# Performance work log

Measured on AMD Instinct MI355X. Metric: run time of the kernel, lower is better.

The kernel has to match this reference:

```python
import jax, jax.numpy as jnp
import numpy as np

BN_EPS = 1e-5

def tanhshrink(x):
    return x - jnp.tanh(x)

def setup_inputs() -> dict:
    key = jax.random.key(0)
    ks = jax.random.split(key, 10)
    B, C, H, W = 32, 128, 32, 32
    RIN, RH, OC = 256, 512, 128
    s = lambda k, shape, fan: jax.random.normal(k, shape, dtype=jnp.float32) * (1.0 / np.sqrt(fan))
    return {
        "x": jax.random.normal(ks[0], (B, C, H, W), dtype=jnp.float32),
        "gamma": jnp.ones((C,), jnp.float32),
        "beta": jnp.zeros((C,), jnp.float32),
        "w_in": s(ks[1], (RIN, C), C),
        "b_in": jnp.zeros((RIN,), jnp.float32),
        "w_ih": s(ks[2], (RH, RIN), RIN),
        "b_ih": jnp.zeros((RH,), jnp.float32),
        "w_hh": s(ks[3], (RH, RH), RH),
        "b_hh": jnp.zeros((RH,), jnp.float32),
        "w_out": s(ks[4], (OC, RH), RH),
        "b_out": jnp.zeros((OC,), jnp.float32),
    }

def reference(x, gamma, beta, w_in, b_in, w_ih, b_ih, w_hh, b_hh, w_out, b_out):
    B, C, H, W = x.shape
    RH = w_hh.shape[0]
    # BatchNorm2d (training mode: batch statistics, biased variance)
    mean = jnp.mean(x, axis=(0, 2, 3), keepdims=True)
    var = jnp.var(x, axis=(0, 2, 3), keepdims=True)
    xn = (x - mean) * jax.lax.rsqrt(var + BN_EPS)
    xn = xn * gamma[None, :, None, None] + beta[None, :, None, None]
    # (B, L, C) sequence of flattened spatial locations
    seq = jnp.transpose(xn, (0, 2, 3, 1)).reshape(B, H * W, C)
    # Per-timestep Linear + Tanhshrink: has no recurrence, batch it over L
    inp = tanhshrink(jnp.einsum('blc,ic->bli', seq, w_in) + b_in)  # (B, L, RIN)
    # Precompute input contribution to RNNCell for all steps
    xgate = jnp.einsum('bli,hi->blh', inp, w_ih) + b_ih + b_hh  # (B, L, RH)
    xgate_t = jnp.transpose(xgate, (1, 0, 2))  # (L, B, RH)

    def step(h, xg):
        h_new = jnp.tanh(xg + h @ w_hh.T)
        return h_new, h_new

    h0 = jnp.zeros((B, RH), x.dtype)
    _, hs = jax.lax.scan(step, h0, xgate_t)  # (L, B, RH)
    outputs = jnp.transpose(hs, (1, 0, 2))  # (B, L, RH)
    out_seq = jnp.einsum('blh,oh->blo', outputs, w_out) + b_out  # (B, L, OC)
    out = jnp.transpose(out_seq.reshape(B, H, W, -1), (0, 3, 1, 2))
    return out
```

## Files before the change

kernel.cpp:

```cpp
#include <hip/hip_runtime.h>
#include <hip/hip_fp16.h>

typedef _Float16 f16;
typedef _Float16 f16x2 __attribute__((ext_vector_type(2)));
typedef _Float16 f16x8 __attribute__((ext_vector_type(8)));
typedef float    f32x4 __attribute__((ext_vector_type(4)));
typedef unsigned int u32;
typedef unsigned long long u64;

#define BN_EPS 1e-5f

static constexpr int BB  = 32;
static constexpr int CC  = 128;
static constexpr int HWN = 1024;
static constexpr int RIN = 256;
static constexpr int RH  = 512;
static constexpr int OCN = 128;

__global__ void bn_stats_kernel(const float* __restrict__ x,
                                const float* __restrict__ gamma,
                                const float* __restrict__ beta,
                                float* __restrict__ scale,
                                float* __restrict__ shift) {
    int c = blockIdx.x;
    int tid = threadIdx.x;
    float s = 0.f, s2 = 0.f;
    const float* xc = x + (size_t)c * HWN;
    for (int idx = tid; idx < BB * HWN; idx += 256) {
        int b = idx >> 10, hw = idx & 1023;
        float v = xc[(size_t)b * (CC * HWN) + hw];
        s += v; s2 += v * v;
    }
    for (int off = 32; off > 0; off >>= 1) {
        s  += __shfl_down(s, off, 64);
        s2 += __shfl_down(s2, off, 64);
    }
    __shared__ float ls[4], ls2[4];
    int wv = tid >> 6, ln = tid & 63;
    if (ln == 0) { ls[wv] = s; ls2[wv] = s2; }
    __syncthreads();
    if (tid == 0) {
        float ts  = ls[0] + ls[1] + ls[2] + ls[3];
        float ts2 = ls2[0] + ls2[1] + ls2[2] + ls2[3];
        const float inv_n = 1.0f / (BB * HWN);
        float mean = ts * inv_n;
        float var  = ts2 * inv_n - mean * mean;
        float rstd = rsqrtf(var + BN_EPS);
        float sc = gamma[c] * rstd;
        scale[c] = sc;
        shift[c] = beta[c] - mean * sc;
    }
}

__global__ void prep_x_kernel(const float* __restrict__ x,
                              const float* __restrict__ scale,
                              const float* __restrict__ shift,
                              f16* __restrict__ A1) {
    __shared__ float tile[32][33];
    int tx = threadIdx.x, ty = threadIdx.y;
    int hb = blockIdx.x, cb = blockIdx.y, b = blockIdx.z;
    #pragma unroll
    for (int k = 0; k < 4; k++) {
        int c  = cb * 32 + ty + 8 * k;
        int hw = hb * 32 + tx;
        tile[ty + 8 * k][tx] = x[(size_t)b * (CC * HWN) + (size_t)c * HWN + hw];
    }
    __syncthreads();
    #pragma unroll
    for (int k = 0; k < 4; k++) {
        int hw = hb * 32 + ty + 8 * k;
        int c  = cb * 32 + tx;
        float v = tile[tx][ty + 8 * k];
        A1[(size_t)(b * HWN + hw) * CC + c] = (f16)(v * scale[c] + shift[c]);
    }
}

__global__ void prep_w_kernel(const float* __restrict__ w_in,
                              const float* __restrict__ w_ih,
                              const float* __restrict__ w_out,
                              const float* __restrict__ w_hh,
                              const float* __restrict__ b_ih,
                              const float* __restrict__ b_hh,
                              f16* __restrict__ w_in_h,
                              f16* __restrict__ w_ih_h,
                              f16* __restrict__ w_out_h,
                              u32* __restrict__ wr,
                              float* __restrict__ bihh,
                              u64* __restrict__ comm) {
    int idx = blockIdx.x * 256 + threadIdx.x;
    if (idx < 32768) { w_in_h[idx] = (f16)w_in[idx]; return; }
    idx -= 32768;
    if (idx < 131072) { w_ih_h[idx] = (f16)w_ih[idx]; return; }
    idx -= 131072;
    if (idx < 65536) { w_out_h[idx] = (f16)w_out[idx]; return; }
    idx -= 65536;
    if (idx < 131072) {
        int s = idx >> 15, rem = idx & 32767;
        int t = rem >> 6, k = rem & 63;
        int r = k >> 4, n = k & 15;
        int jg = t & 31, sl = t >> 5;
        int j  = s * 128 + 4 * jg + r;
        int i2 = sl * 16 + n;
        f16 lo = (f16)w_hh[(size_t)j * 512 + 2 * i2];
        f16 hi = (f16)w_hh[(size_t)j * 512 + 2 * i2 + 1];
        wr[idx] = (u32)__builtin_bit_cast(unsigned short, lo) |
                  ((u32)__builtin_bit_cast(unsigned short, hi) << 16);
        return;
    }
    idx -= 131072;
    if (idx < 512) { bihh[idx] = b_ih[idx] + b_hh[idx]; return; }
    idx -= 512;
    if (idx < 16384) comm[idx] = 0ULL;
}

template <int MODE>
__global__ void gemm_kernel(const f16* __restrict__ A,
                            const f16* __restrict__ W,
                            const float* __restrict__ bias,
                            void* __restrict__ outp,
                            int N, int K) {
    int wave = threadIdx.x >> 6;
    int lane = threadIdx.x & 63;
    int q = lane >> 4, r = lane & 15;
    int bm = blockIdx.x * 256 + wave * 64;
    int bn = blockIdx.y * 64;

    f32x4 acc[4][4];
    #pragma unroll
    for (int i = 0; i < 4; i++)
        #pragma unroll
        for (int j = 0; j < 4; j++)
            acc[i][j] = (f32x4){0.f, 0.f, 0.f, 0.f};

    const f16* Ap = A + (size_t)(bm + r) * K + 8 * q;
    const f16* Wp = W + (size_t)(bn + r) * K + 8 * q;

    for (int k = 0; k < K; k += 32) {
        f16x8 av[4], bv[4];
        #pragma unroll
        for (int i = 0; i < 4; i++)
            av[i] = *(const f16x8*)(Ap + (size_t)(16 * i) * K + k);
        #pragma unroll
        for (int i = 0; i < 4; i++)
            bv[i] = *(const f16x8*)(Wp + (size_t)(16 * i) * K + k);
        #pragma unroll
        for (int mi = 0; mi < 4; mi++)
            #pragma unroll
            for (int ni = 0; ni < 4; ni++)
                acc[mi][ni] = __builtin_amdgcn_mfma_f32_16x16x32_f16(
                    av[mi], bv[ni], acc[mi][ni], 0, 0, 0);
    }

    #pragma unroll
    for (int mi = 0; mi < 4; mi++) {
        #pragma unroll
        for (int ni = 0; ni < 4; ni++) {
            int col = bn + 16 * ni + r;
            float bval = bias[col];
            #pragma unroll
            for (int i = 0; i < 4; i++) {
                int row = bm + 16 * mi + 4 * q + i;
                float val = acc[mi][ni][i] + bval;
                if (MODE == 0) {
                    val = val - tanhf(val);
                    ((f16*)outp)[(size_t)row * N + col] = (f16)val;
                } else if (MODE == 1) {
                    ((f16*)outp)[(size_t)row * N + col] = (f16)val;
                } else {
                    int b = row >> 10, hw = row & 1023;
                    ((float*)outp)[(size_t)b * (OCN * HWN) + (size_t)col * HWN + hw] = val;
                }
            }
        }
    }
}

__device__ __forceinline__ float dot2acc(u32 w, f16x2 h, float c) {
#if __has_builtin(__builtin_amdgcn_fdot2)
    return __builtin_amdgcn_fdot2(__builtin_bit_cast(f16x2, w), h, c, false);
#else
    f16x2 a = __builtin_bit_cast(f16x2, w);
    return c + (float)a[0] * (float)h[0] + (float)a[1] * (float)h[1];
#endif
}

#define ROW16(acc, WA, WB, WC, WD)                                  \
    acc = dot2acc(WA.x, H0,  acc); acc = dot2acc(WA.y, H1,  acc);   \
    acc = dot2acc(WA.z, H2,  acc); acc = dot2acc(WA.w, H3,  acc);   \
    acc = dot2acc(WB.x, H4,  acc); acc = dot2acc(WB.y, H5,  acc);   \
    acc = dot2acc(WB.z, H6,  acc); acc = dot2acc(WB.w, H7,  acc);   \
    acc = dot2acc(WC.x, H8,  acc); acc = dot2acc(WC.y, H9,  acc);   \
    acc = dot2acc(WC.z, H10, acc); acc = dot2acc(WC.w, H11, acc);   \
    acc = dot2acc(WD.x, H12, acc); acc = dot2acc(WD.y, H13, acc);   \
    acc = dot2acc(WD.z, H14, acc); acc = dot2acc(WD.w, H15, acc)

__global__ __launch_bounds__(512, 2) void rnn_kernel(const u32* WR,
                                                     f16* __restrict__ xh,
                                                     u64* comm) {
    const int wg = blockIdx.x;
    const int b  = wg & 31;
    const int s  = wg >> 5;
    const int t  = threadIdx.x;
    const int jg = t & 31;
    const int sl = t >> 5;

    __shared__ __align__(16) f16 hbuf[512];
    __shared__ float part[16][128];

    unsigned long long wpa =
        (unsigned long long)(WR + ((size_t)(s * 512 + t) << 6));
    asm volatile("" : "+v"(wpa));
    const uint4* wp = (const uint4*)wpa;
    uint4 W0 = wp[0],  W1 = wp[1],  W2 = wp[2],  W3 = wp[3];
    uint4 W4 = wp[4],  W5 = wp[5],  W6 = wp[6],  W7 = wp[7];
    uint4 W8 = wp[8],  W9 = wp[9],  W10 = wp[10], W11 = wp[11];
    uint4 W12 = wp[12], W13 = wp[13], W14 = wp[14], W15 = wp[15];

    if (t < 256) ((u32*)hbuf)[t] = 0u;
    __syncthreads();

    f16* xb = xh + (size_t)b * (HWN * RH) + s * 128;
    float xnext = 0.f;
    if (t < 128) xnext = (float)xb[t];

    u64* cb = comm + (size_t)b * 256;
    const uint4* hq = (const uint4*)hbuf;

    for (int step = 0; step < HWN; step++) {
        float xcur = xnext;
        if (t < 128 && step + 1 < HWN)
            xnext = (float)xb[(size_t)(step + 1) * RH + t];

        uint4 q0 = hq[sl*4+0], q1 = hq[sl*4+1], q2 = hq[sl*4+2], q3 = hq[sl*4+3];
        f16x2 H0  = __builtin_bit_cast(f16x2, q0.x), H1  = __builtin_bit_cast(f16x2, q0.y);
        f16x2 H2  = __builtin_bit_cast(f16x2, q0.z), H3  = __builtin_bit_cast(f16x2, q0.w);
        f16x2 H4  = __builtin_bit_cast(f16x2, q1.x), H5  = __builtin_bit_cast(f16x2, q1.y);
        f16x2 H6  = __builtin_bit_cast(f16x2, q1.z), H7  = __builtin_bit_cast(f16x2, q1.w);
        f16x2 H8  = __builtin_bit_cast(f16x2, q2.x), H9  = __builtin_bit_cast(f16x2, q2.y);
        f16x2 H10 = __builtin_bit_cast(f16x2, q2.z), H11 = __builtin_bit_cast(f16x2, q2.w);
        f16x2 H12 = __builtin_bit_cast(f16x2, q3.x), H13 = __builtin_bit_cast(f16x2, q3.y);
        f16x2 H14 = __builtin_bit_cast(f16x2, q3.z), H15 = __builtin_bit_cast(f16x2, q3.w);
        float a0 = 0.f, a1 = 0.f, a2 = 0.f, a3 = 0.f;
        ROW16(a0, W0,  W1,  W2,  W3);
        ROW16(a1, W4,  W5,  W6,  W7);
        ROW16(a2, W8,  W9,  W10, W11);
        ROW16(a3, W12, W13, W14, W15);
        *(f32x4*)&part[sl][4 * jg] = (f32x4){a0, a1, a2, a3};
        __syncthreads();

        const u32 tag = (u32)(step + 1);
        const size_t pbase = (size_t)(tag & 1) * 8192;

        if (t >= 256 && t < 448) {
            int pi = (t - 256) >> 6;
            int widx = t & 63;
            int p = pi + (pi >= s ? 1 : 0);
            u64* addr = &cb[pbase + p * 64 + widx];
            u64 v  = __hip_atomic_load(addr, __ATOMIC_RELAXED, __HIP_MEMORY_SCOPE_AGENT);
            u64 v2 = __hip_atomic_load(addr, __ATOMIC_RELAXED, __HIP_MEMORY_SCOPE_AGENT);
            int guard = 0;
            while ((u32)(v >> 32) != tag && ++guard < (1 << 17)) {
                v = v2;
                v2 = __hip_atomic_load(addr, __ATOMIC_RELAXED, __HIP_MEMORY_SCOPE_AGENT);
            }
            ((u32*)hbuf)[p * 64 + widx] = (u32)v;
        }
        if (t < 128) {
            float y = xcur;
            #pragma unroll
            for (int k = 0; k < 16; k++) y += part[k][t];
            float h = tanhf(y);
            f16 hf = (f16)h;
            u32 hu = (u32)__builtin_bit_cast(unsigned short, hf);
            u32 other = (u32)__shfl_down((int)hu, 1, 64);
            if ((t & 1) == 0) {
                u64 v = ((u64)tag << 32) | (u64)(hu | (other << 16));
                __hip_atomic_store(&cb[pbase + s * 64 + (t >> 1)], v,
                                   __ATOMIC_RELAXED, __HIP_MEMORY_SCOPE_AGENT);
            }
            hbuf[s * 128 + t] = hf;
            xb[(size_t)step * RH + t] = hf;
        }
        __syncthreads();
    }
}

extern "C" void kernel_launch(void* const* d_in, const int* in_sizes, int n_in,
                              void* d_out, int out_size, void* d_ws, size_t ws_size,
                              hipStream_t stream) {
    const float* x     = (const float*)d_in[0];
    const float* gamma = (const float*)d_in[1];
    const float* beta  = (const float*)d_in[2];
    const float* w_in  = (const float*)d_in[3];
    const float* b_in  = (const float*)d_in[4];
    const float* w_ih  = (const float*)d_in[5];
    const float* b_ih  = (const float*)d_in[6];
    const float* w_hh  = (const float*)d_in[7];
    const float* b_hh  = (const float*)d_in[8];
    const float* w_out = (const float*)d_in[9];
    const float* b_out = (const float*)d_in[10];

    char* ws = (char*)d_ws;
    float* scale   = (float*)(ws + 0);
    float* shift   = (float*)(ws + 512);
    float* bihh    = (float*)(ws + 1024);
    f16*   w_in_h  = (f16*)(ws + 4096);
    f16*   w_ih_h  = (f16*)(ws + 69632);
    f16*   w_out_h = (f16*)(ws + 331776);
    u32*   wr      = (u32*)(ws + 462848);
    u64*   comm    = (u64*)(ws + 987136);
    f16*   xh      = (f16*)(ws + 1179648);
    f16*   A1      = (f16*)(ws + 34734080);
    f16*   inp     = (f16*)(ws + 43122688);

    bn_stats_kernel<<<128, 256, 0, stream>>>(x, gamma, beta, scale, shift);
    prep_w_kernel<<<1474, 256, 0, stream>>>(w_in, w_ih, w_out, w_hh, b_ih, b_hh,
                                            w_in_h, w_ih_h, w_out_h, wr, bihh, comm);
    prep_x_kernel<<<dim3(32, 4, 32), dim3(32, 8), 0, stream>>>(x, scale, shift, A1);
    gemm_kernel<0><<<dim3(128, 4), 256, 0, stream>>>(A1, w_in_h, b_in, (void*)inp, RIN, CC);
    gemm_kernel<1><<<dim3(128, 8), 256, 0, stream>>>(inp, w_ih_h, bihh, (void*)xh, RH, RIN);
    rnn_kernel<<<128, 512, 0, stream>>>(wr, xh, comm);
    gemm_kernel<2><<<dim3(128, 2), 256, 0, stream>>>(xh, w_out_h, b_out, d_out, OCN, RH);
}
```

Before: 1.601 ms.

## Split RNN hidden dim across 8 workgroups per batch with shuffle reductions

The recurrent kernel moves from 4 to 8 workgroups per batch row (256 total), each owning 64 hidden units. The weights are stored in an XOR-swizzled layout so that 8 lanes share a row and reduce their partials with xor-shuffles, which removes the shared-memory partial-sum array and one barrier per step. The hidden state is double-buffered in LDS, the exchange packs one fp16 value plus a 16-bit tag into a 32-bit word, and the first poll load is issued before the dot products to hide latency. In exchange each step needs more cross-workgroup communication, since 7 peers are polled instead of 3, and 256 co-resident workgroups are required for the spin-waits to make progress.

After: 1.653 ms. +3.2%, slower.

```diff
diff --git a/kernel.cpp b/kernel.cpp
--- a/kernel.cpp
+++ b/kernel.cpp
@@ -86,7 +86,7 @@
                               f16* __restrict__ w_out_h,
                               u32* __restrict__ wr,
                               float* __restrict__ bihh,
-                              u64* __restrict__ comm) {
+                              u32* __restrict__ comm) {
     int idx = blockIdx.x * 256 + threadIdx.x;
     if (idx < 32768) { w_in_h[idx] = (f16)w_in[idx]; return; }
     idx -= 32768;
@@ -95,12 +95,12 @@
     if (idx < 65536) { w_out_h[idx] = (f16)w_out[idx]; return; }
     idx -= 65536;
     if (idx < 131072) {
-        int s = idx >> 15, rem = idx & 32767;
-        int t = rem >> 6, k = rem & 63;
-        int r = k >> 4, n = k & 15;
-        int jg = t & 31, sl = t >> 5;
-        int j  = s * 128 + 4 * jg + r;
-        int i2 = sl * 16 + n;
+        int s = idx >> 14, rem = idx & 16383;
+        int t = rem >> 5, w = rem & 31;
+        int r = t >> 3, c = t & 7;
+        int i = w >> 2, k = w & 3;
+        int i2 = c * 32 + 4 * (i ^ c) + k;
+        int j  = s * 64 + r;
         f16 lo = (f16)w_hh[(size_t)j * 512 + 2 * i2];
         f16 hi = (f16)w_hh[(size_t)j * 512 + 2 * i2 + 1];
         wr[idx] = (u32)__builtin_bit_cast(unsigned short, lo) |
@@ -110,7 +110,7 @@
     idx -= 131072;
     if (idx < 512) { bihh[idx] = b_ih[idx] + b_hh[idx]; return; }
     idx -= 512;
-    if (idx < 16384) comm[idx] = 0ULL;
+    if (idx < 32768) comm[idx] = 0u;
 }
 
 template <int MODE>
@@ -184,102 +184,113 @@
 #endif
 }
 
-#define ROW16(acc, WA, WB, WC, WD)                                  \
-    acc = dot2acc(WA.x, H0,  acc); acc = dot2acc(WA.y, H1,  acc);   \
-    acc = dot2acc(WA.z, H2,  acc); acc = dot2acc(WA.w, H3,  acc);   \
-    acc = dot2acc(WB.x, H4,  acc); acc = dot2acc(WB.y, H5,  acc);   \
-    acc = dot2acc(WB.z, H6,  acc); acc = dot2acc(WB.w, H7,  acc);   \
-    acc = dot2acc(WC.x, H8,  acc); acc = dot2acc(WC.y, H9,  acc);   \
-    acc = dot2acc(WC.z, H10, acc); acc = dot2acc(WC.w, H11, acc);   \
-    acc = dot2acc(WD.x, H12, acc); acc = dot2acc(WD.y, H13, acc);   \
-    acc = dot2acc(WD.z, H14, acc); acc = dot2acc(WD.w, H15, acc)
-
-__global__ __launch_bounds__(512, 2) void rnn_kernel(const u32* WR,
-                                                     f16* __restrict__ xh,
-                                                     u64* comm) {
+__device__ __forceinline__ f16x2 u2h(u32 w) { return __builtin_bit_cast(f16x2, w); }
+
+__global__ void __launch_bounds__(512)
+__attribute__((amdgpu_waves_per_eu(2, 2)))
+rnn_kernel(const u32* WR, f16* __restrict__ xh, u32* comm) {
     const int wg = blockIdx.x;
     const int b  = wg & 31;
     const int s  = wg >> 5;
     const int t  = threadIdx.x;
-    const int jg = t & 31;
-    const int sl = t >> 5;
-
-    __shared__ __align__(16) f16 hbuf[512];
-    __shared__ float part[16][128];
-
-    unsigned long long wpa =
-        (unsigned long long)(WR + ((size_t)(s * 512 + t) << 6));
-    asm volatile("" : "+v"(wpa));
-    const uint4* wp = (const uint4*)wpa;
-    uint4 W0 = wp[0],  W1 = wp[1],  W2 = wp[2],  W3 = wp[3];
-    uint4 W4 = wp[4],  W5 = wp[5],  W6 = wp[6],  W7 = wp[7];
-    uint4 W8 = wp[8],  W9 = wp[9],  W10 = wp[10], W11 = wp[11];
-    uint4 W12 = wp[12], W13 = wp[13], W14 = wp[14], W15 = wp[15];
-
-    if (t < 256) ((u32*)hbuf)[t] = 0u;
+    const int r  = t >> 3;
+    const int c  = t & 7;
+    const bool leader = (c == 0);
+
+    __shared__ __align__(16) f16 hbuf[2][512];
+
+    const uint4* wp = (const uint4*)(WR + ((size_t)(s * 512 + t) << 5));
+    uint4 q0_ = wp[0], q1_ = wp[1], q2_ = wp[2], q3_ = wp[3];
+    uint4 q4_ = wp[4], q5_ = wp[5], q6_ = wp[6], q7_ = wp[7];
+    u32 W00 = q0_.x, W01 = q0_.y, W02 = q0_.z, W03 = q0_.w;
+    u32 W04 = q1_.x, W05 = q1_.y, W06 = q1_.z, W07 = q1_.w;
+    u32 W08 = q2_.x, W09 = q2_.y, W10 = q2_.z, W11 = q2_.w;
+    u32 W12 = q3_.x, W13 = q3_.y, W14 = q3_.z, W15 = q3_.w;
+    u32 W16 = q4_.x, W17 = q4_.y, W18 = q4_.z, W19 = q4_.w;
+    u32 W20 = q5_.x, W21 = q5_.y, W22 = q5_.z, W23 = q5_.w;
+    u32 W24 = q6_.x, W25 = q6_.y, W26 = q6_.z, W27 = q6_.w;
+    u32 W28 = q7_.x, W29 = q7_.y, W30 = q7_.z, W31 = q7_.w;
+    asm volatile("" : "+v"(W00), "+v"(W01), "+v"(W02), "+v"(W03),
+                      "+v"(W04), "+v"(W05), "+v"(W06), "+v"(W07),
+                      "+v"(W08), "+v"(W09), "+v"(W10), "+v"(W11),
+                      "+v"(W12), "+v"(W13), "+v"(W14), "+v"(W15));
+    asm volatile("" : "+v"(W16), "+v"(W17), "+v"(W18), "+v"(W19),
+                      "+v"(W20), "+v"(W21), "+v"(W22), "+v"(W23),
+                      "+v"(W24), "+v"(W25), "+v"(W26), "+v"(W27),
+                      "+v"(W28), "+v"(W29), "+v"(W30), "+v"(W31));
+
+    ((u32*)hbuf)[t] = 0u;
     __syncthreads();
 
-    f16* xb = xh + (size_t)b * (HWN * RH) + s * 128;
-    float xnext = 0.f;
-    if (t < 128) xnext = (float)xb[t];
-
-    u64* cb = comm + (size_t)b * 256;
-    const uint4* hq = (const uint4*)hbuf;
+    f16* xg = xh + (size_t)b * (HWN * RH) + s * 64 + r;
+    float xnext = leader ? (float)xg[0] : 0.f;
+
+    const bool isPoller = (t >= 64);
+    const int pi = (t - 64) >> 6;
+    const int pp = pi + (pi >= s ? 1 : 0);
+    const int pj = t & 63;
+
+    const char* hb0 = (const char*)&hbuf[0][0];
+    const int cbyte = c << 7;
 
     for (int step = 0; step < HWN; step++) {
+        const u32 tag  = (u32)(step + 1);
+        const int nxt  = (int)(tag & 1);
+        const char* hb = hb0 + ((step & 1) << 10);
+
+        u32* paddr = comm + ((size_t)(tag & 1) << 14) + ((size_t)b << 9)
+                          + (pp << 6) + pj;
+        u32 vpre = 0;
+        if (isPoller)
+            vpre = __hip_atomic_load(paddr, __ATOMIC_RELAXED, __HIP_MEMORY_SCOPE_AGENT);
+
         float xcur = xnext;
-        if (t < 128 && step + 1 < HWN)
-            xnext = (float)xb[(size_t)(step + 1) * RH + t];
-
-        uint4 q0 = hq[sl*4+0], q1 = hq[sl*4+1], q2 = hq[sl*4+2], q3 = hq[sl*4+3];
-        f16x2 H0  = __builtin_bit_cast(f16x2, q0.x), H1  = __builtin_bit_cast(f16x2, q0.y);
-        f16x2 H2  = __builtin_bit_cast(f16x2, q0.z), H3  = __builtin_bit_cast(f16x2, q0.w);
-        f16x2 H4  = __builtin_bit_cast(f16x2, q1.x), H5  = __builtin_bit_cast(f16x2, q1.y);
-        f16x2 H6  = __builtin_bit_cast(f16x2, q1.z), H7  = __builtin_bit_cast(f16x2, q1.w);
-        f16x2 H8  = __builtin_bit_cast(f16x2, q2.x), H9  = __builtin_bit_cast(f16x2, q2.y);
-        f16x2 H10 = __builtin_bit_cast(f16x2, q2.z), H11 = __builtin_bit_cast(f16x2, q2.w);
-        f16x2 H12 = __builtin_bit_cast(f16x2, q3.x), H13 = __builtin_bit_cast(f16x2, q3.y);
-        f16x2 H14 = __builtin_bit_cast(f16x2, q3.z), H15 = __builtin_bit_cast(f16x2, q3.w);
-        float a0 = 0.f, a1 = 0.f, a2 = 0.f, a3 = 0.f;
-        ROW16(a0, W0,  W1,  W2,  W3);
-        ROW16(a1, W4,  W5,  W6,  W7);
-        ROW16(a2, W8,  W9,  W10, W11);
-        ROW16(a3, W12, W13, W14, W15);
-        *(f32x4*)&part[sl][4 * jg] = (f32x4){a0, a1, a2, a3};
-        __syncthreads();
-
-        const u32 tag = (u32)(step + 1);
-        const size_t pbase = (size_t)(tag & 1) * 8192;
-
-        if (t >= 256 && t < 448) {
-            int pi = (t - 256) >> 6;
-            int widx = t & 63;
-            int p = pi + (pi >= s ? 1 : 0);
-            u64* addr = &cb[pbase + p * 64 + widx];
-            u64 v  = __hip_atomic_load(addr, __ATOMIC_RELAXED, __HIP_MEMORY_SCOPE_AGENT);
-            u64 v2 = __hip_atomic_load(addr, __ATOMIC_RELAXED, __HIP_MEMORY_SCOPE_AGENT);
-            int guard = 0;
-            while ((u32)(v >> 32) != tag && ++guard < (1 << 17)) {
-                v = v2;
-                v2 = __hip_atomic_load(addr, __ATOMIC_RELAXED, __HIP_MEMORY_SCOPE_AGENT);
+        if (leader && step + 1 < HWN)
+            xnext = (float)xg[(size_t)(step + 1) * RH];
+
+        float aA = 0.f, aB = 0.f, aC = 0.f, aD = 0.f;
+        #define GRP(i, ACC, Wa, Wb, Wc, Wd)                                   \
+        {   uint4 q = *(const uint4*)(hb + (cbyte | (((i) ^ c) << 4)));       \
+            ACC = dot2acc(Wa, u2h(q.x), ACC);                                 \
+            ACC = dot2acc(Wb, u2h(q.y), ACC);                                 \
+            ACC = dot2acc(Wc, u2h(q.z), ACC);                                 \
+            ACC = dot2acc(Wd, u2h(q.w), ACC); }
+        GRP(0, aA, W00, W01, W02, W03)
+        GRP(1, aB, W04, W05, W06, W07)
+        GRP(2, aC, W08, W09, W10, W11)
+        GRP(3, aD, W12, W13, W14, W15)
+        GRP(4, aA, W16, W17, W18, W19)
+        GRP(5, aB, W20, W21, W22, W23)
+        GRP(6, aC, W24, W25, W26, W27)
+        GRP(7, aD, W28, W29, W30, W31)
+        #undef GRP
+        float acc = (aA + aB) + (aC + aD);
+        acc += __shfl_xor(acc, 1, 64);
+        acc += __shfl_xor(acc, 2, 64);
+        acc += __shfl_xor(acc, 4, 64);
+
+        if (leader) {
+            float h = tanhf(xcur + acc);
+            f16 hf = (f16)h;
+            u32 word = (tag << 16) | (u32)__builtin_bit_cast(unsigned short, hf);
+            __hip_atomic_store(comm + ((size_t)(tag & 1) << 14) + ((size_t)b << 9)
+                                    + (s << 6) + r,
+                               word, __ATOMIC_RELAXED, __HIP_MEMORY_SCOPE_AGENT);
+            hbuf[nxt][(s << 6) + r] = hf;
+            xg[(size_t)step * RH] = hf;
+        }
+        if (isPoller) {
+            u32 v = vpre;
+            if ((v >> 16) != tag) {
+                u32 v2 = __hip_atomic_load(paddr, __ATOMIC_RELAXED, __HIP_MEMORY_SCOPE_AGENT);
+                int guard = 0;
+                while ((v >> 16) != tag && ++guard < (1 << 17)) {
+                    v = v2;
+                    v2 = __hip_atomic_load(paddr, __ATOMIC_RELAXED, __HIP_MEMORY_SCOPE_AGENT);
+                }
             }
-            ((u32*)hbuf)[p * 64 + widx] = (u32)v;
-        }
-        if (t < 128) {
-            float y = xcur;
-            #pragma unroll
-            for (int k = 0; k < 16; k++) y += part[k][t];
-            float h = tanhf(y);
-            f16 hf = (f16)h;
-            u32 hu = (u32)__builtin_bit_cast(unsigned short, hf);
-            u32 other = (u32)__shfl_down((int)hu, 1, 64);
-            if ((t & 1) == 0) {
-                u64 v = ((u64)tag << 32) | (u64)(hu | (other << 16));
-                __hip_atomic_store(&cb[pbase + s * 64 + (t >> 1)], v,
-                                   __ATOMIC_RELAXED, __HIP_MEMORY_SCOPE_AGENT);
-            }
-            hbuf[s * 128 + t] = hf;
-            xb[(size_t)step * RH + t] = hf;
+            hbuf[nxt][(pp << 6) + pj] =
+                __builtin_bit_cast(f16, (unsigned short)(v & 0xFFFFu));
         }
         __syncthreads();
     }
@@ -308,17 +319,17 @@
     f16*   w_ih_h  = (f16*)(ws + 69632);
     f16*   w_out_h = (f16*)(ws + 331776);
     u32*   wr      = (u32*)(ws + 462848);
-    u64*   comm    = (u64*)(ws + 987136);
+    u32*   comm    = (u32*)(ws + 987136);
     f16*   xh      = (f16*)(ws + 1179648);
     f16*   A1      = (f16*)(ws + 34734080);
     f16*   inp     = (f16*)(ws + 43122688);
 
     bn_stats_kernel<<<128, 256, 0, stream>>>(x, gamma, beta, scale, shift);
-    prep_w_kernel<<<1474, 256, 0, stream>>>(w_in, w_ih, w_out, w_hh, b_ih, b_hh,
+    prep_w_kernel<<<1538, 256, 0, stream>>>(w_in, w_ih, w_out, w_hh, b_ih, b_hh,
                                             w_in_h, w_ih_h, w_out_h, wr, bihh, comm);
     prep_x_kernel<<<dim3(32, 4, 32), dim3(32, 8), 0, stream>>>(x, scale, shift, A1);
     gemm_kernel<0><<<dim3(128, 4), 256, 0, stream>>>(A1, w_in_h, b_in, (void*)inp, RIN, CC);
     gemm_kernel<1><<<dim3(128, 8), 256, 0, stream>>>(inp, w_ih_h, bihh, (void*)xh, RH, RIN);
-    rnn_kernel<<<128, 512, 0, stream>>>(wr, xh, comm);
+    rnn_kernel<<<256, 512, 0, stream>>>(wr, xh, comm);
     gemm_kernel<2><<<dim3(128, 2), 256, 0, stream>>>(xh, w_out_h, b_out, d_out, OCN, RH);
 }
```
